# Kernel optimization log

Hardware: AMD Instinct MI355X
Metric: run time of the kernel (lower is better)

The kernel has to match this reference:

```python
import jax, jax.numpy as jnp
import numpy as np

NUM_HEAD = 16
DIM = 1024
T, B = 2048, 4


def setup_inputs() -> dict:
    key = jax.random.key(0)
    ks = jax.random.split(key, 12)
    s = 1.0 / np.sqrt(DIM)
    return {
        "x1": jax.random.normal(ks[0], (T, B, DIM), jnp.float32),
        "x2": jax.random.normal(ks[1], (T, B, DIM), jnp.float32),
        "Wq": jax.random.normal(ks[2], (DIM, DIM), jnp.float32) * s,
        "bq": jax.random.normal(ks[3], (DIM,), jnp.float32) * 0.01,
        "Wk": jax.random.normal(ks[4], (DIM, DIM), jnp.float32) * s,
        "bk": jax.random.normal(ks[5], (DIM,), jnp.float32) * 0.01,
        "Wv": jax.random.normal(ks[6], (DIM, DIM), jnp.float32) * s,
        "bv": jax.random.normal(ks[7], (DIM,), jnp.float32) * 0.01,
        "Wu": jax.random.normal(ks[8], (DIM, DIM), jnp.float32) * s,
        "bu": jax.random.normal(ks[9], (DIM,), jnp.float32) * 0.01,
    }


def reference(x1, x2, Wq, bq, Wk, bk, Wv, bv, Wu, bu):
    T1, B1, C = x1.shape
    T2 = x2.shape[0]
    H = NUM_HEAD
    hd = C // H
    # (T,B,C) -> (B,T,C)
    x1b = jnp.transpose(x1, (1, 0, 2))
    x2b = jnp.transpose(x2, (1, 0, 2))
    # torch Linear: y = x @ W.T + b
    q = (x1b @ Wq.T + bq).reshape(B1, T1, H, hd).transpose(0, 2, 1, 3)  # (B,H,T1,hd)
    k = (x2b @ Wk.T + bk).reshape(B1, T2, H, hd).transpose(0, 2, 1, 3)
    v = (x2b @ Wv.T + bv).reshape(B1, T2, H, hd).transpose(0, 2, 1, 3)
    # NOTE: source scales by 1/sqrt(C) (full dim), not 1/sqrt(head_dim)
    attn = jnp.einsum("bhqd,bhkd->bhqk", q, k) / jnp.sqrt(jnp.asarray(C, q.dtype))
    attn = jax.nn.softmax(attn, axis=-1)
    # dropout = identity (eval mode, deterministic reference)
    out = jnp.einsum("bhqk,bhkd->bhqd", attn, v)  # (B,H,T1,hd)
    out = out.transpose(0, 2, 1, 3).reshape(B1, T1, C)  # merge heads
    out = out @ Wu.T + bu
    return out
```

## Files before the change

### kernel.cpp

```cpp
#include <hip/hip_runtime.h>

#define TSEQ 2048
#define BB 4
#define CDIM 1024
#define NH 16
#define HD 64
#define MR (TSEQ*BB)
#define C2SCALE 0.045084220f

typedef __attribute__((ext_vector_type(8))) short sh8;
typedef __attribute__((ext_vector_type(4))) short sh4;
typedef __attribute__((ext_vector_type(4))) float f4;
typedef __attribute__((ext_vector_type(4))) unsigned int u32x4;

__device__ __forceinline__ unsigned short f2bf(float x){
  unsigned u = __builtin_bit_cast(unsigned, x);
  u += 0x7fffu + ((u>>16)&1u);
  return (unsigned short)(u>>16);
}

__device__ __forceinline__ unsigned cvtpk(float a, float b){
  unsigned r;
  asm("v_cvt_pk_bf16_f32 %0, %1, %2" : "=v"(r) : "v"(a), "v"(b));
  return r;
}

__device__ __forceinline__ void gll16(const unsigned short* g, unsigned short* l){
  __builtin_amdgcn_global_load_lds(
      (const __attribute__((address_space(1))) unsigned int*)g,
      (__attribute__((address_space(3))) unsigned int*)l, 16, 0, 0);
}

__global__ void conv_x(const float* __restrict__ a, const float* __restrict__ b,
                       unsigned short* __restrict__ ya, unsigned short* __restrict__ yb){
  const float* s = blockIdx.y ? b : a;
  unsigned short* d = blockIdx.y ? yb : ya;
  int i = (blockIdx.x*256 + threadIdx.x)*4;
  f4 v = *(const f4*)(s+i);
  sh4 o;
  o.x = (short)f2bf(v.x); o.y = (short)f2bf(v.y);
  o.z = (short)f2bf(v.z); o.w = (short)f2bf(v.w);
  *(sh4*)(d+i) = o;
}

__global__ void conv_w(const float* __restrict__ w0, const float* __restrict__ w1,
                       const float* __restrict__ w2, const float* __restrict__ w3,
                       unsigned short* __restrict__ y0, unsigned short* __restrict__ y1,
                       unsigned short* __restrict__ y2, unsigned short* __restrict__ y3){
  const float* s; unsigned short* d;
  switch(blockIdx.y){
    case 0: s=w0; d=y0; break;
    case 1: s=w1; d=y1; break;
    case 2: s=w2; d=y2; break;
    default: s=w3; d=y3; break;
  }
  int i = (blockIdx.x*256 + threadIdx.x)*4;
  f4 v = *(const f4*)(s+i);
  sh4 o;
  o.x = (short)f2bf(v.x); o.y = (short)f2bf(v.y);
  o.z = (short)f2bf(v.z); o.w = (short)f2bf(v.w);
  *(sh4*)(d+i) = o;
}

#define NKT4 16
#define BUFS4 24576

__device__ __forceinline__ void gemm_core4(
    const unsigned short* __restrict__ Aglob, const unsigned short* __restrict__ Bglob,
    unsigned short* smem, int m0, int n0, int tid, f4 (&acc)[8][4])
{
  const int wave = tid>>6, lane = tid&63;
  const int g = lane>>4, c = lane&15;
  const int wr = wave>>1, wc = wave&1;

  const int srow = tid>>3, sch = tid&7;
  const unsigned short* aBase = Aglob + (size_t)(m0+srow)*CDIM + (sch^(srow&7))*8;
  const unsigned short* bBase = Bglob + (size_t)(n0+srow)*CDIM + (sch^(srow&7))*8;

#pragma unroll
  for (int i=0;i<8;i++) gll16(aBase + (size_t)i*32*CDIM,      smem + (i*256+tid)*8);
#pragma unroll
  for (int i=0;i<4;i++) gll16(bBase + (size_t)i*32*CDIM,      smem + 16384 + (i*256+tid)*8);
#pragma unroll
  for (int i=0;i<8;i++) gll16(aBase + (size_t)i*32*CDIM + 64, smem + BUFS4 + (i*256+tid)*8);
#pragma unroll
  for (int i=0;i<4;i++) gll16(bBase + (size_t)i*32*CDIM + 64, smem + BUFS4 + 16384 + (i*256+tid)*8);
  asm volatile("s_waitcnt vmcnt(12)" ::: "memory");
  __builtin_amdgcn_s_barrier();

  const int arow = wr*128 + c;
  const int brow = wc*64 + c;
  const int ch0 = g ^ (c&7);
  const int ch1 = (4+g) ^ (c&7);

  int q = 0;
  for (int kt=0; kt<NKT4; kt++){
    unsigned short* bufc = smem + q*BUFS4;
    int rr = q+2; if (rr>=3) rr-=3;
    unsigned short* dst = smem + rr*BUFS4;
    if (kt+2 < NKT4){
      const size_t koff = (size_t)(kt+2)*64;
#pragma unroll
      for (int i=0;i<8;i++) gll16(aBase + (size_t)i*32*CDIM + koff, dst + (i*256+tid)*8);
#pragma unroll
      for (int i=0;i<4;i++) gll16(bBase + (size_t)i*32*CDIM + koff, dst + 16384 + (i*256+tid)*8);
    }
    sh8 af[8][2], bfr[4][2];
#pragma unroll
    for (int mt=0;mt<8;mt++){
      af[mt][0] = *(const sh8*)(bufc + (arow+mt*16)*64 + ch0*8);
      af[mt][1] = *(const sh8*)(bufc + (arow+mt*16)*64 + ch1*8);
    }
#pragma unroll
    for (int nt=0;nt<4;nt++){
      bfr[nt][0] = *(const sh8*)(bufc + 16384 + (brow+nt*16)*64 + ch0*8);
      bfr[nt][1] = *(const sh8*)(bufc + 16384 + (brow+nt*16)*64 + ch1*8);
    }
    __builtin_amdgcn_s_setprio(1);
#pragma unroll
    for (int mt=0;mt<8;mt++)
#pragma unroll
      for (int nt=0;nt<4;nt++){
        acc[mt][nt] = __builtin_amdgcn_mfma_f32_16x16x32_bf16(af[mt][0], bfr[nt][0], acc[mt][nt],0,0,0);
        acc[mt][nt] = __builtin_amdgcn_mfma_f32_16x16x32_bf16(af[mt][1], bfr[nt][1], acc[mt][nt],0,0,0);
      }
    __builtin_amdgcn_s_setprio(0);
    if (kt < NKT4-1){
      if (kt < NKT4-2) asm volatile("s_waitcnt vmcnt(12)" ::: "memory");
      else             asm volatile("s_waitcnt vmcnt(0)" ::: "memory");
    }
    __builtin_amdgcn_s_barrier();
    q = (q==2)?0:q+1;
  }
}

__global__ __launch_bounds__(256,1) void gemm_u(
    const unsigned short* __restrict__ A, const unsigned short* __restrict__ Bw,
    const float* __restrict__ bias, float* __restrict__ Cout){
  __shared__ unsigned short smem[3*BUFS4];
  const int tid  = threadIdx.x;
  const int wave = tid>>6, lane = tid&63;
  const int g = lane>>4, c = lane&15;
  const int m0 = blockIdx.x*256, n0 = blockIdx.y*128;
  const int wr = wave>>1, wc = wave&1;
  f4 acc[8][4] = {};
  gemm_core4(A, Bw, smem, m0, n0, tid, acc);

#pragma unroll
  for (int nt=0; nt<4; nt++){
    int nn = n0 + wc*64 + nt*16 + c;
    float bsv = bias[nn];
#pragma unroll
    for (int mt=0; mt<8; mt++){
      int mb = m0 + wr*128 + mt*16 + 4*g;
#pragma unroll
      for (int r=0; r<4; r++)
        Cout[(size_t)(mb+r)*CDIM + nn] = acc[mt][nt][r] + bsv;
    }
  }
}

#define NKT 16
#define TBUF 32768

__device__ __forceinline__ void gemm_core8(
    const unsigned short* __restrict__ Aglob, const unsigned short* __restrict__ Bglob,
    unsigned short* smem, int m0, int n0, int tid, f4 (&acc)[8][4])
{
  const int lane = tid&63;
  const int g = lane>>4, c = lane&15;
  const int wv = tid>>6;
  const int wr = wv>>2, wcn = wv&3;

  const int rloc = tid>>3, cho = tid&7;
  const int aside = (rloc>>5)<<7;
  const int ar = (rloc&31) + aside;
  const int schk = (cho ^ (rloc&7))*8;
  const unsigned short* aS = Aglob + (size_t)(m0+ar)*CDIM + schk;
  const unsigned short* bS = Bglob + (size_t)(n0+rloc)*CDIM + schk;
  const int aD = ar*64 + cho*8;
  const int bD = 16384 + rloc*64 + cho*8;

#define STA(k2,q) gll16(aS + (size_t)(q)*32*CDIM + (k2)*64, smem + ((k2)&1)*TBUF + (q)*2048 + aD)
#define STB(k2,q) gll16(bS + (size_t)(q)*64*CDIM + (k2)*64, smem + ((k2)&1)*TBUF + (q)*4096 + bD)

  const int ch0 = (g ^ (c&7))*8;
  const int ch1 = ((4+g) ^ (c&7))*8;
  const int arow0 = (wr*128 + c)*64;
  const int brow0 = 16384 + (wcn*64 + c)*64;

#pragma unroll
  for (int q=0;q<4;q++) STA(0,q);
#pragma unroll
  for (int q=0;q<4;q++) STB(0,q);
#pragma unroll
  for (int q=0;q<3;q++){ STA(1,q); STB(1,q); }
  asm volatile("s_waitcnt vmcnt(6)" ::: "memory");
  __builtin_amdgcn_s_barrier();

  for (int kt=0; kt<NKT; kt++){
    const unsigned short* bufA = smem + (kt&1)*TBUF;
    sh8 bfr[4][2];
#pragma unroll
    for (int p=0; p<4; p++){
      sh8 af[2][2];
#pragma unroll
      for (int i=0;i<2;i++){
        af[i][0] = *(const sh8*)(bufA + arow0 + (2*p+i)*1024 + ch0);
        af[i][1] = *(const sh8*)(bufA + arow0 + (2*p+i)*1024 + ch1);
      }
      if (p==0){
#pragma unroll
        for (int nt=0;nt<4;nt++){
          bfr[nt][0] = *(const sh8*)(bufA + brow0 + nt*1024 + ch0);
          bfr[nt][1] = *(const sh8*)(bufA + brow0 + nt*1024 + ch1);
        }
      }
      if (p==0){
        if (kt+1 < NKT){ STA(kt+1,3); STB(kt+1,3); }
      } else {
        if (kt+2 < NKT){ STA(kt+2,p-1); STB(kt+2,p-1); }
      }
      __builtin_amdgcn_s_barrier();
      __builtin_amdgcn_s_setprio(1);
#pragma unroll
      for (int i=0;i<2;i++)
#pragma unroll
        for (int nt=0;nt<4;nt++){
          acc[2*p+i][nt] = __builtin_amdgcn_mfma_f32_16x16x32_bf16(af[i][0], bfr[nt][0], acc[2*p+i][nt],0,0,0);
          acc[2*p+i][nt] = __builtin_amdgcn_mfma_f32_16x16x32_bf16(af[i][1], bfr[nt][1], acc[2*p+i][nt],0,0,0);
        }
      __builtin_amdgcn_s_setprio(0);
      if (p==3){
        if (kt < NKT-2)       asm volatile("s_waitcnt vmcnt(6)" ::: "memory");
        else if (kt == NKT-2) asm volatile("s_waitcnt vmcnt(0)" ::: "memory");
      }
      __builtin_amdgcn_s_barrier();
    }
  }
#undef STA
#undef STB
}

__global__ __launch_bounds__(512,2) void gemm_qkv(
    const unsigned short* __restrict__ x1b, const unsigned short* __restrict__ x2b,
    const unsigned short* __restrict__ wq, const unsigned short* __restrict__ wk,
    const unsigned short* __restrict__ wv,
    const float* __restrict__ bq, const float* __restrict__ bk, const float* __restrict__ bv,
    unsigned short* __restrict__ Qo, unsigned short* __restrict__ Ko,
    unsigned short* __restrict__ Vo){
  __shared__ unsigned short smem[2*TBUF];
  const int z = blockIdx.z;
  const unsigned short* A  = (z==0) ? x1b : x2b;
  const unsigned short* Bw = (z==0) ? wq : (z==1) ? wk : wv;
  const float* bias        = (z==0) ? bq : (z==1) ? bk : bv;
  const int tid  = threadIdx.x;
  const int lane = tid&63;
  const int g = lane>>4, c = lane&15;
  const int wv2 = tid>>6;
  const int wr = wv2>>2, wcn = wv2&3;
  const int m0 = blockIdx.x*256, n0 = blockIdx.y*256;
  f4 acc[8][4] = {};
  gemm_core8(A, Bw, smem, m0, n0, tid, acc);

  if (z != 2){
#pragma unroll
    for (int nt=0; nt<4; nt++){
      int nn = n0 + wcn*64 + nt*16 + c;
      float bsv = bias[nn];
#pragma unroll
      for (int mt=0; mt<8; mt++){
        int mb = m0 + wr*128 + mt*16 + 4*g;
#pragma unroll
        for (int r=0; r<4; r++){
          float v = acc[mt][nt][r] + bsv;
          int mm = mb + r;
          if (z==0) Qo[(size_t)mm*CDIM + nn] = f2bf(v*C2SCALE);
          else      Ko[(size_t)mm*CDIM + nn] = f2bf(v);
        }
      }
    }
  } else {
    unsigned short* lv = smem;
#pragma unroll
    for (int nt=0; nt<4; nt++){
      int nl = wcn*64 + nt*16 + c;
      float bsv = bias[n0 + nl];
      int key = (nl&7)<<3;
#pragma unroll
      for (int mt=0; mt<8; mt++){
        int tl = wr*32 + mt*4 + g;
        int pos = nl*256 + (tl ^ key);
#pragma unroll
        for (int r=0; r<4; r++)
          lv[pos + r*64] = f2bf(acc[mt][nt][r] + bsv);
      }
    }
    __builtin_amdgcn_s_barrier();
    const int j = tid&7;
#pragma unroll
    for (int it=0; it<16; it++){
      int rid = it*64 + (tid>>3);
      int nl = rid>>2, bb = rid&3;
      sh8 vrow = *(const sh8*)(lv + nl*256 + bb*64 + ((j ^ (nl&7))<<3));
      int nn = n0 + nl; int h = nn>>6, d = nn&63;
      *(sh8*)(Vo + ((size_t)(bb*NH + h)*HD + d)*TSEQ + (m0>>2) + j*8) = vrow;
    }
  }
}

__global__ __launch_bounds__(256,4) void attn_kernel(
    const unsigned short* __restrict__ Q, const unsigned short* __restrict__ Kb,
    const unsigned short* __restrict__ Vt, unsigned short* __restrict__ O){
  __shared__ unsigned short Ks[2][64*64];
  __shared__ unsigned short Vs[2][64*64];
  const int tid=threadIdx.x, wave=tid>>6, lane=tid&63;
  const int g=lane>>4, c=lane&15;
  const bool godd = (g&1);
  const int gx = blockIdx.x;
  const int bh = ((gx>>7)<<3) | (gx&7);
  const int qt = (gx>>3)&15;
  const int b = bh>>4, h = bh&15;
  const int qbase = qt*128 + wave*32;

  const unsigned short* kb0[2];
  const unsigned short* vb0[2];
#pragma unroll
  for (int i=0; i<2; i++){
    int cc = i*256+tid;
    int krow = cc>>3, kch = (cc&7) ^ (krow&7);
    kb0[i] = Kb + ((size_t)krow*BB + b)*CDIM + h*HD + kch*8;
    int vd = cc>>3, vch = (cc&7) ^ (vd&7);
    vb0[i] = Vt + ((size_t)(b*NH+h)*HD + vd)*TSEQ + vch*8;
  }

  sh8 qfr[2][2];
#pragma unroll
  for (int qf=0; qf<2; qf++)
#pragma unroll
    for (int kc=0; kc<2; kc++){
      int t = qbase + qf*16 + c;
      qfr[qf][kc] = *(const sh8*)(Q + ((size_t)t*BB + b)*CDIM + h*HD + kc*32 + g*8);
    }

  f4 oacc[4][2] = {};
  float lrun[2] = {0.f, 0.f};

#pragma unroll
  for (int i=0; i<2; i++){
    gll16(kb0[i], Ks[0] + (i*256+tid)*8);
    gll16(vb0[i], Vs[0] + (i*256+tid)*8);
  }
  __syncthreads();

  const int NT = TSEQ/64;
  int cur = 0;
  for (int it=0; it<NT; it++){
    if (it+1 < NT){
      int k0n = (it+1)*64;
#pragma unroll
      for (int i=0; i<2; i++){
        gll16(kb0[i] + (size_t)k0n*BB*CDIM, Ks[cur^1] + (i*256+tid)*8);
        gll16(vb0[i] + k0n,                 Vs[cur^1] + (i*256+tid)*8);
      }
    }
    const unsigned short* ks = Ks[cur];
    const unsigned short* vs = Vs[cur];

#pragma unroll
    for (int sub=0; sub<2; sub++){
      f4 sacc[2][2] = {};
      __builtin_amdgcn_s_setprio(1);
#pragma unroll
      for (int j=0; j<2; j++){
        int kf = sub*2 + j;
        sh8 af[2];
#pragma unroll
        for (int kc=0; kc<2; kc++){
          int ch = (kc*4+g) ^ (c&7);
          af[kc] = *(const sh8*)(ks + (kf*16+c)*64 + ch*8);
        }
#pragma unroll
        for (int kc=0; kc<2; kc++)
#pragma unroll
          for (int qf=0; qf<2; qf++)
            sacc[j][qf] = __builtin_amdgcn_mfma_f32_16x16x32_bf16(af[kc], qfr[qf][kc], sacc[j][qf],0,0,0);
      }
      __builtin_amdgcn_s_setprio(0);

      sh8 pf[2];
#pragma unroll
      for (int qf=0; qf<2; qf++){
        f4 sa = sacc[0][qf];
        f4 sb = sacc[1][qf];
        float pa0 = __builtin_amdgcn_exp2f(sa[0]);
        float pa1 = __builtin_amdgcn_exp2f(sa[1]);
        float pa2 = __builtin_amdgcn_exp2f(sa[2]);
        float pa3 = __builtin_amdgcn_exp2f(sa[3]);
        float pb0 = __builtin_amdgcn_exp2f(sb[0]);
        float pb1 = __builtin_amdgcn_exp2f(sb[1]);
        float pb2 = __builtin_amdgcn_exp2f(sb[2]);
        float pb3 = __builtin_amdgcn_exp2f(sb[3]);
        lrun[qf] += ((pa0+pa1)+(pa2+pa3)) + ((pb0+pb1)+(pb2+pb3));
        unsigned A0 = cvtpk(pa0, pa1);
        unsigned A1 = cvtpk(pa2, pa3);
        unsigned B0 = cvtpk(pb0, pb1);
        unsigned B1 = cvtpk(pb2, pb3);
        asm("v_permlane32_swap_b32 %0, %1" : "+v"(A0), "+v"(B0));
        asm("v_permlane32_swap_b32 %0, %1" : "+v"(A1), "+v"(B1));
        unsigned xA0 = (unsigned)__builtin_amdgcn_ds_swizzle((int)A0, 0x401F);
        unsigned xA1 = (unsigned)__builtin_amdgcn_ds_swizzle((int)A1, 0x401F);
        unsigned xB0 = (unsigned)__builtin_amdgcn_ds_swizzle((int)B0, 0x401F);
        unsigned xB1 = (unsigned)__builtin_amdgcn_ds_swizzle((int)B1, 0x401F);
        u32x4 pw;
        pw.x = godd ? xB0 : A0;
        pw.y = godd ? xB1 : A1;
        pw.z = godd ? B0  : xA0;
        pw.w = godd ? B1  : xA1;
        pf[qf] = __builtin_bit_cast(sh8, pw);
      }
      __builtin_amdgcn_s_setprio(1);
#pragma unroll
      for (int df=0; df<4; df++){
        int ch = (sub*4+g) ^ (c&7);
        sh8 vf = *(const sh8*)(vs + (df*16+c)*64 + ch*8);
#pragma unroll
        for (int qf=0; qf<2; qf++)
          oacc[df][qf] = __builtin_amdgcn_mfma_f32_16x16x32_bf16(vf, pf[qf], oacc[df][qf],0,0,0);
      }
      __builtin_amdgcn_s_setprio(0);
    }

    __syncthreads();
    cur ^= 1;
  }

#pragma unroll
  for (int qf=0; qf<2; qf++){
    lrun[qf] += __shfl_xor(lrun[qf], 16, 64);
    lrun[qf] += __shfl_xor(lrun[qf], 32, 64);
    float inv = 1.0f/lrun[qf];
    int t = qbase + qf*16 + c;
#pragma unroll
    for (int df=0; df<4; df++){
      uint2 pr;
      pr.x = cvtpk(oacc[df][qf][0]*inv, oacc[df][qf][1]*inv);
      pr.y = cvtpk(oacc[df][qf][2]*inv, oacc[df][qf][3]*inv);
      *(uint2*)(O + ((size_t)b*TSEQ + t)*CDIM + h*HD + df*16 + 4*g) = pr;
    }
  }
}

extern "C" void kernel_launch(void* const* d_in, const int* in_sizes, int n_in,
                              void* d_out, int out_size, void* d_ws, size_t ws_size,
                              hipStream_t stream){
  (void)in_sizes; (void)n_in; (void)out_size; (void)ws_size;
  const float* x1 = (const float*)d_in[0];
  const float* x2 = (const float*)d_in[1];
  const float* Wq = (const float*)d_in[2];
  const float* bq = (const float*)d_in[3];
  const float* Wk = (const float*)d_in[4];
  const float* bk = (const float*)d_in[5];
  const float* Wv = (const float*)d_in[6];
  const float* bv = (const float*)d_in[7];
  const float* Wu = (const float*)d_in[8];
  const float* bu = (const float*)d_in[9];

  unsigned short* ws = (unsigned short*)d_ws;
  size_t o = 0;
  unsigned short* x1b = ws + o; o += (size_t)MR*CDIM;
  unsigned short* x2b = ws + o; o += (size_t)MR*CDIM;
  unsigned short* wqb = ws + o; o += (size_t)CDIM*CDIM;
  unsigned short* wkb = ws + o; o += (size_t)CDIM*CDIM;
  unsigned short* wvb = ws + o; o += (size_t)CDIM*CDIM;
  unsigned short* wub = ws + o; o += (size_t)CDIM*CDIM;
  unsigned short* Qb  = ws + o; o += (size_t)MR*CDIM;
  unsigned short* Kbf = ws + o; o += (size_t)MR*CDIM;
  unsigned short* Vtb = ws + o; o += (size_t)MR*CDIM;
  unsigned short* Ob  = x1b;

  conv_x<<<dim3((MR*CDIM)/1024, 2),   256, 0, stream>>>(x1, x2, x1b, x2b);
  conv_w<<<dim3((CDIM*CDIM)/1024, 4), 256, 0, stream>>>(Wq, Wk, Wv, Wu, wqb, wkb, wvb, wub);

  gemm_qkv<<<dim3(MR/256, CDIM/256, 3), 512, 0, stream>>>(
      x1b, x2b, wqb, wkb, wvb, bq, bk, bv, Qb, Kbf, Vtb);
  attn_kernel<<<dim3(1024), 256, 0, stream>>>(Qb, Kbf, Vtb, Ob);
  gemm_u<<<dim3(MR/256, CDIM/128), 256, 0, stream>>>(Ob, wub, bu, (float*)d_out);
}
```

Before: 308.5 us.

## Replace QKV GEMM core with 256x128 K32 double-buffer and enlarge attention query tile

The QKV projection kernel drops its 512-thread 256x256 tile, which used a 64-wide K step and a deep multi-stage prefetch. It now uses a 256-thread 256x128 tile with a 32-wide K step, a simple double buffer and less shared memory, so more blocks can be resident; the V transpose epilogue is split into two halves to fit the smaller buffer. The attention kernel now gives each wave 64 queries instead of 32, halving the grid and reusing each K/V tile across more queries. That attention change doubles accumulator registers and lowers occupancy to 2 blocks. The simpler GEMM pipeline also loses overlap and issues a barrier every small K step.

```diff
diff --git a/kernel.cpp b/kernel.cpp
--- a/kernel.cpp
+++ b/kernel.cpp
@@ -160,113 +160,93 @@
   }
 }
 
-#define NKT 16
-#define TBUF 32768
-
-__device__ __forceinline__ void gemm_core8(
+#define QNST 32
+#define QSLOT 12288
+
+__device__ __forceinline__ void gemm_core32(
     const unsigned short* __restrict__ Aglob, const unsigned short* __restrict__ Bglob,
     unsigned short* smem, int m0, int n0, int tid, f4 (&acc)[8][4])
 {
-  const int lane = tid&63;
+  const int wave = tid>>6, lane = tid&63;
   const int g = lane>>4, c = lane&15;
-  const int wv = tid>>6;
-  const int wr = wv>>2, wcn = wv&3;
-
-  const int rloc = tid>>3, cho = tid&7;
-  const int aside = (rloc>>5)<<7;
-  const int ar = (rloc&31) + aside;
-  const int schk = (cho ^ (rloc&7))*8;
-  const unsigned short* aS = Aglob + (size_t)(m0+ar)*CDIM + schk;
-  const unsigned short* bS = Bglob + (size_t)(n0+rloc)*CDIM + schk;
-  const int aD = ar*64 + cho*8;
-  const int bD = 16384 + rloc*64 + cho*8;
-
-#define STA(k2,q) gll16(aS + (size_t)(q)*32*CDIM + (k2)*64, smem + ((k2)&1)*TBUF + (q)*2048 + aD)
-#define STB(k2,q) gll16(bS + (size_t)(q)*64*CDIM + (k2)*64, smem + ((k2)&1)*TBUF + (q)*4096 + bD)
-
-  const int ch0 = (g ^ (c&7))*8;
-  const int ch1 = ((4+g) ^ (c&7))*8;
-  const int arow0 = (wr*128 + c)*64;
-  const int brow0 = 16384 + (wcn*64 + c)*64;
-
-#pragma unroll
-  for (int q=0;q<4;q++) STA(0,q);
-#pragma unroll
-  for (int q=0;q<4;q++) STB(0,q);
-#pragma unroll
-  for (int q=0;q<3;q++){ STA(1,q); STB(1,q); }
-  asm volatile("s_waitcnt vmcnt(6)" ::: "memory");
-  __builtin_amdgcn_s_barrier();
-
-  for (int kt=0; kt<NKT; kt++){
-    const unsigned short* bufA = smem + (kt&1)*TBUF;
-    sh8 bfr[4][2];
-#pragma unroll
-    for (int p=0; p<4; p++){
-      sh8 af[2][2];
-#pragma unroll
-      for (int i=0;i<2;i++){
-        af[i][0] = *(const sh8*)(bufA + arow0 + (2*p+i)*1024 + ch0);
-        af[i][1] = *(const sh8*)(bufA + arow0 + (2*p+i)*1024 + ch1);
-      }
-      if (p==0){
-#pragma unroll
-        for (int nt=0;nt<4;nt++){
-          bfr[nt][0] = *(const sh8*)(bufA + brow0 + nt*1024 + ch0);
-          bfr[nt][1] = *(const sh8*)(bufA + brow0 + nt*1024 + ch1);
-        }
-      }
-      if (p==0){
-        if (kt+1 < NKT){ STA(kt+1,3); STB(kt+1,3); }
-      } else {
-        if (kt+2 < NKT){ STA(kt+2,p-1); STB(kt+2,p-1); }
-      }
-      __builtin_amdgcn_s_barrier();
-      __builtin_amdgcn_s_setprio(1);
-#pragma unroll
-      for (int i=0;i<2;i++)
-#pragma unroll
-        for (int nt=0;nt<4;nt++){
-          acc[2*p+i][nt] = __builtin_amdgcn_mfma_f32_16x16x32_bf16(af[i][0], bfr[nt][0], acc[2*p+i][nt],0,0,0);
-          acc[2*p+i][nt] = __builtin_amdgcn_mfma_f32_16x16x32_bf16(af[i][1], bfr[nt][1], acc[2*p+i][nt],0,0,0);
-        }
-      __builtin_amdgcn_s_setprio(0);
-      if (p==3){
-        if (kt < NKT-2)       asm volatile("s_waitcnt vmcnt(6)" ::: "memory");
-        else if (kt == NKT-2) asm volatile("s_waitcnt vmcnt(0)" ::: "memory");
-      }
-      __builtin_amdgcn_s_barrier();
-    }
-  }
-#undef STA
-#undef STB
-}
-
-__global__ __launch_bounds__(512,2) void gemm_qkv(
+  const int wr = wave>>1, wc = wave&1;
+
+  const unsigned short* aSrc[4]; int aOff[4];
+  const unsigned short* bSrc[2]; int bOff[2];
+#pragma unroll
+  for (int i=0;i<4;i++){
+    int slot = i*256+tid; int row = slot>>2, ch = slot&3;
+    aSrc[i] = Aglob + (size_t)(m0+row)*CDIM + (ch ^ ((row>>1)&3))*8;
+    aOff[i] = slot*8;
+  }
+#pragma unroll
+  for (int i=0;i<2;i++){
+    int slot = i*256+tid; int row = slot>>2, ch = slot&3;
+    bSrc[i] = Bglob + (size_t)(n0+row)*CDIM + (ch ^ ((row>>1)&3))*8;
+    bOff[i] = 8192 + slot*8;
+  }
+  const int swz = (c>>1)&3;
+  const int aro = (wr*128 + c)*32 + (g ^ swz)*8;
+  const int bro = 8192 + (wc*64 + c)*32 + (g ^ swz)*8;
+
+#pragma unroll
+  for (int i=0;i<4;i++) gll16(aSrc[i], smem + aOff[i]);
+#pragma unroll
+  for (int i=0;i<2;i++) gll16(bSrc[i], smem + bOff[i]);
+  __syncthreads();
+
+  int cur = 0;
+  for (int s=0; s<QNST; s++){
+    if (s+1 < QNST){
+      const int ko = (s+1)*32;
+      unsigned short* dst = smem + (cur^1)*QSLOT;
+#pragma unroll
+      for (int i=0;i<4;i++) gll16(aSrc[i]+ko, dst + aOff[i]);
+#pragma unroll
+      for (int i=0;i<2;i++) gll16(bSrc[i]+ko, dst + bOff[i]);
+    }
+    const unsigned short* bufc = smem + cur*QSLOT;
+    sh8 bfr[4];
+#pragma unroll
+    for (int nt=0;nt<4;nt++) bfr[nt] = *(const sh8*)(bufc + bro + nt*512);
+    __builtin_amdgcn_s_setprio(1);
+#pragma unroll
+    for (int mt=0;mt<8;mt++){
+      sh8 af = *(const sh8*)(bufc + aro + mt*512);
+#pragma unroll
+      for (int nt=0;nt<4;nt++)
+        acc[mt][nt] = __builtin_amdgcn_mfma_f32_16x16x32_bf16(af, bfr[nt], acc[mt][nt],0,0,0);
+    }
+    __builtin_amdgcn_s_setprio(0);
+    __syncthreads();
+    cur ^= 1;
+  }
+}
+
+__global__ __launch_bounds__(256,3) void gemm_qkv(
     const unsigned short* __restrict__ x1b, const unsigned short* __restrict__ x2b,
     const unsigned short* __restrict__ wq, const unsigned short* __restrict__ wk,
     const unsigned short* __restrict__ wv,
     const float* __restrict__ bq, const float* __restrict__ bk, const float* __restrict__ bv,
     unsigned short* __restrict__ Qo, unsigned short* __restrict__ Ko,
     unsigned short* __restrict__ Vo){
-  __shared__ unsigned short smem[2*TBUF];
+  __shared__ unsigned short smem[2*QSLOT];
   const int z = blockIdx.z;
   const unsigned short* A  = (z==0) ? x1b : x2b;
   const unsigned short* Bw = (z==0) ? wq : (z==1) ? wk : wv;
   const float* bias        = (z==0) ? bq : (z==1) ? bk : bv;
   const int tid  = threadIdx.x;
-  const int lane = tid&63;
+  const int wave = tid>>6, lane = tid&63;
   const int g = lane>>4, c = lane&15;
-  const int wv2 = tid>>6;
-  const int wr = wv2>>2, wcn = wv2&3;
-  const int m0 = blockIdx.x*256, n0 = blockIdx.y*256;
+  const int m0 = blockIdx.x*256, n0 = blockIdx.y*128;
+  const int wr = wave>>1, wc = wave&1;
   f4 acc[8][4] = {};
-  gemm_core8(A, Bw, smem, m0, n0, tid, acc);
+  gemm_core32(A, Bw, smem, m0, n0, tid, acc);
 
   if (z != 2){
 #pragma unroll
     for (int nt=0; nt<4; nt++){
-      int nn = n0 + wcn*64 + nt*16 + c;
+      int nn = n0 + wc*64 + nt*16 + c;
       float bsv = bias[nn];
 #pragma unroll
       for (int mt=0; mt<8; mt++){
@@ -283,33 +263,40 @@
   } else {
     unsigned short* lv = smem;
 #pragma unroll
-    for (int nt=0; nt<4; nt++){
-      int nl = wcn*64 + nt*16 + c;
-      float bsv = bias[n0 + nl];
-      int key = (nl&7)<<3;
-#pragma unroll
-      for (int mt=0; mt<8; mt++){
-        int tl = wr*32 + mt*4 + g;
-        int pos = nl*256 + (tl ^ key);
-#pragma unroll
-        for (int r=0; r<4; r++)
-          lv[pos + r*64] = f2bf(acc[mt][nt][r] + bsv);
-      }
-    }
-    __builtin_amdgcn_s_barrier();
-    const int j = tid&7;
-#pragma unroll
-    for (int it=0; it<16; it++){
-      int rid = it*64 + (tid>>3);
-      int nl = rid>>2, bb = rid&3;
-      sh8 vrow = *(const sh8*)(lv + nl*256 + bb*64 + ((j ^ (nl&7))<<3));
-      int nn = n0 + nl; int h = nn>>6, d = nn&63;
-      *(sh8*)(Vo + ((size_t)(bb*NH + h)*HD + d)*TSEQ + (m0>>2) + j*8) = vrow;
-    }
-  }
-}
-
-__global__ __launch_bounds__(256,4) void attn_kernel(
+    for (int h2=0; h2<2; h2++){
+      __builtin_amdgcn_s_barrier();
+      if (wr == h2){
+#pragma unroll
+        for (int nt=0; nt<4; nt++){
+          int nl = wc*64 + nt*16 + c;
+          float bsv = bias[n0 + nl];
+          int key = (nl&3)<<3;
+#pragma unroll
+          for (int mt=0; mt<8; mt++){
+            int mloc = mt*16 + 4*g;
+#pragma unroll
+            for (int r=0; r<4; r++){
+              int m2 = mloc + r;
+              lv[nl*128 + (m2&3)*32 + ((m2>>2) ^ key)] = f2bf(acc[mt][nt][r] + bsv);
+            }
+          }
+        }
+      }
+      __builtin_amdgcn_s_barrier();
+      const int j = tid&3;
+#pragma unroll
+      for (int it=0; it<8; it++){
+        int rid = it*64 + (tid>>2);
+        int nl = rid>>2, bb = rid&3;
+        sh8 vrow = *(const sh8*)(lv + nl*128 + bb*32 + ((j ^ (nl&3))*8));
+        int nn = n0 + nl; int hh = nn>>6, dd = nn&63;
+        *(sh8*)(Vo + ((size_t)(bb*NH + hh)*HD + dd)*TSEQ + ((m0 + h2*128)>>2) + j*8) = vrow;
+      }
+    }
+  }
+}
+
+__global__ __launch_bounds__(256,2) void attn_kernel(
     const unsigned short* __restrict__ Q, const unsigned short* __restrict__ Kb,
     const unsigned short* __restrict__ Vt, unsigned short* __restrict__ O){
   __shared__ unsigned short Ks[2][64*64];
@@ -318,10 +305,10 @@
   const int g=lane>>4, c=lane&15;
   const bool godd = (g&1);
   const int gx = blockIdx.x;
-  const int bh = ((gx>>7)<<3) | (gx&7);
-  const int qt = (gx>>3)&15;
+  const int bh = ((gx>>6)<<3) | (gx&7);
+  const int qt = (gx>>3)&7;
   const int b = bh>>4, h = bh&15;
-  const int qbase = qt*128 + wave*32;
+  const int qbase = qt*256 + wave*64;
 
   const unsigned short* kb0[2];
   const unsigned short* vb0[2];
@@ -334,17 +321,17 @@
     vb0[i] = Vt + ((size_t)(b*NH+h)*HD + vd)*TSEQ + vch*8;
   }
 
-  sh8 qfr[2][2];
-#pragma unroll
-  for (int qf=0; qf<2; qf++)
+  sh8 qfr[4][2];
+#pragma unroll
+  for (int qf=0; qf<4; qf++)
 #pragma unroll
     for (int kc=0; kc<2; kc++){
       int t = qbase + qf*16 + c;
       qfr[qf][kc] = *(const sh8*)(Q + ((size_t)t*BB + b)*CDIM + h*HD + kc*32 + g*8);
     }
 
-  f4 oacc[4][2] = {};
-  float lrun[2] = {0.f, 0.f};
+  f4 oacc[4][4] = {};
+  float lrun[4] = {0.f, 0.f, 0.f, 0.f};
 
 #pragma unroll
   for (int i=0; i<2; i++){
@@ -369,7 +356,7 @@
 
 #pragma unroll
     for (int sub=0; sub<2; sub++){
-      f4 sacc[2][2] = {};
+      f4 sacc[2][4] = {};
       __builtin_amdgcn_s_setprio(1);
 #pragma unroll
       for (int j=0; j<2; j++){
@@ -383,14 +370,14 @@
 #pragma unroll
         for (int kc=0; kc<2; kc++)
 #pragma unroll
-          for (int qf=0; qf<2; qf++)
+          for (int qf=0; qf<4; qf++)
             sacc[j][qf] = __builtin_amdgcn_mfma_f32_16x16x32_bf16(af[kc], qfr[qf][kc], sacc[j][qf],0,0,0);
       }
       __builtin_amdgcn_s_setprio(0);
 
-      sh8 pf[2];
-#pragma unroll
-      for (int qf=0; qf<2; qf++){
+      sh8 pf[4];
+#pragma unroll
+      for (int qf=0; qf<4; qf++){
         f4 sa = sacc[0][qf];
         f4 sb = sacc[1][qf];
         float pa0 = __builtin_amdgcn_exp2f(sa[0]);
@@ -425,7 +412,7 @@
         int ch = (sub*4+g) ^ (c&7);
         sh8 vf = *(const sh8*)(vs + (df*16+c)*64 + ch*8);
 #pragma unroll
-        for (int qf=0; qf<2; qf++)
+        for (int qf=0; qf<4; qf++)
           oacc[df][qf] = __builtin_amdgcn_mfma_f32_16x16x32_bf16(vf, pf[qf], oacc[df][qf],0,0,0);
       }
       __builtin_amdgcn_s_setprio(0);
@@ -436,7 +423,7 @@
   }
 
 #pragma unroll
-  for (int qf=0; qf<2; qf++){
+  for (int qf=0; qf<4; qf++){
     lrun[qf] += __shfl_xor(lrun[qf], 16, 64);
     lrun[qf] += __shfl_xor(lrun[qf], 32, 64);
     float inv = 1.0f/lrun[qf];
@@ -482,8 +469,8 @@
   conv_x<<<dim3((MR*CDIM)/1024, 2),   256, 0, stream>>>(x1, x2, x1b, x2b);
   conv_w<<<dim3((CDIM*CDIM)/1024, 4), 256, 0, stream>>>(Wq, Wk, Wv, Wu, wqb, wkb, wvb, wub);
 
-  gemm_qkv<<<dim3(MR/256, CDIM/256, 3), 512, 0, stream>>>(
+  gemm_qkv<<<dim3(MR/256, CDIM/128, 3), 256, 0, stream>>>(
       x1b, x2b, wqb, wkb, wvb, bq, bk, bv, Qb, Kbf, Vtb);
-  attn_kernel<<<dim3(1024), 256, 0, stream>>>(Qb, Kbf, Vtb, Ob);
+  attn_kernel<<<dim3(512), 256, 0, stream>>>(Qb, Kbf, Vtb, Ob);
   gemm_u<<<dim3(MR/256, CDIM/128), 256, 0, stream>>>(Ob, wub, bu, (float*)d_out);
 }
```

Result: slower. 325.8 us (+5.6%).
